# Kernel tuning notes

Measured on AMD Instinct MI355X. Metric: run time of the kernel, lower is better.

## Reference

```python
import jax, jax.numpy as jnp
import numpy as np

B, S, E = 20, 4096, 256
BLOCK = 128
LEFT, RIGHT = 1, 1


def setup_inputs() -> dict:
    key = jax.random.key(0)
    ks = jax.random.split(key, 6)
    x = jax.random.normal(ks[0], (B, S, E), dtype=jnp.float32)
    scale = 0.02
    Wq = jax.random.normal(ks[1], (E, E), dtype=jnp.float32) * scale
    Wk = jax.random.normal(ks[2], (E, E), dtype=jnp.float32) * scale
    Wv = jax.random.normal(ks[3], (E, E), dtype=jnp.float32) * scale
    Wo = jax.random.normal(ks[4], (E, E), dtype=jnp.float32) * scale
    bo = jnp.zeros((E,), dtype=jnp.float32)
    return {"x": x, "Wq": Wq, "Wk": Wk, "Wv": Wv, "Wo": Wo, "bo": bo}


def _block_context(blocks, left, right):
    # blocks: [B, nb, bs, E] -> [B, nb, (left+right+1)*bs, E]
    b, nb, bs, e = blocks.shape
    w = left + right + 1
    padded = jnp.pad(blocks, ((0, 0), (left, right), (0, 0), (0, 0)))
    idx = jnp.arange(nb)[:, None] + jnp.arange(w)[None, :]  # [nb, w]
    ctx = padded[:, idx]  # [B, nb, w, bs, E]
    return ctx.reshape(b, nb, w * bs, e)


def reference(x, Wq, Wk, Wv, Wo, bo):
    b, s, e = x.shape
    nb = s // BLOCK
    q = x @ Wq
    k = x @ Wk
    v = x @ Wv
    qb = q.reshape(b, nb, BLOCK, e)
    kb = k.reshape(b, nb, BLOCK, e)
    vb = v.reshape(b, nb, BLOCK, e)
    kc = _block_context(kb, LEFT, RIGHT)  # [B, nb, ctx, E]
    vc = _block_context(vb, LEFT, RIGHT)
    logits = jnp.einsum('bnqd,bnkd->bnqk', qb, kc) / jnp.sqrt(jnp.float32(e))
    attn = jax.nn.softmax(logits, axis=-1)
    out = jnp.einsum('bnqk,bnkd->bnqd', attn, vc)  # [B, nb, bs, E]
    # Faithful to TF: TensorArray.stack() -> [nb, B, bs, E], then reshape to [B, S, E]
    out = jnp.transpose(out, (1, 0, 2, 3)).reshape(b, s, e)
    return out @ Wo + bo
```

## Files before the change

kernel.cpp:

```cpp
#include <hip/hip_runtime.h>
#include <stdint.h>

#define B_   20
#define S_   4096
#define E_   256
#define NB_  32
#define M_   (B_ * S_)

#define OFF_Q   41943040ull
#define OFF_K   83886080ull
#define OFF_V   125829120ull
#define OFF_WT  167772160ull

typedef __attribute__((ext_vector_type(4))) float f32x4;
typedef __attribute__((ext_vector_type(8))) short short8;
typedef __attribute__((ext_vector_type(4))) float float4v;
typedef __attribute__((ext_vector_type(4))) unsigned short us4;

__device__ __forceinline__ unsigned short f2bf(float f) {
  unsigned int u = __builtin_bit_cast(unsigned int, f);
  u += 0x7FFFu + ((u >> 16) & 1u);
  return (unsigned short)(u >> 16);
}

__device__ __forceinline__ void glds16(const void* g, void* l) {
  __builtin_amdgcn_global_load_lds(
      (const __attribute__((address_space(1))) unsigned int*)g,
      (__attribute__((address_space(3))) unsigned int*)l, 16, 0, 0);
}

__global__ void k_convert_x(const float* __restrict__ x, unsigned short* __restrict__ xb) {
  size_t id = (size_t)blockIdx.x * 256 + threadIdx.x;
  float4v v = *(const float4v*)(x + id * 4);
  us4 o;
  o[0] = f2bf(v[0]); o[1] = f2bf(v[1]); o[2] = f2bf(v[2]); o[3] = f2bf(v[3]);
  *(us4*)(xb + id * 4) = o;
}

__global__ void k_convert_w(const float* __restrict__ Wq, const float* __restrict__ Wk,
                            const float* __restrict__ Wv, const float* __restrict__ Wo,
                            unsigned short* __restrict__ WT) {
  const float* src = (blockIdx.x == 0) ? Wq : (blockIdx.x == 1) ? Wk
                   : (blockIdx.x == 2) ? Wv : Wo;
  unsigned short* dst = WT + (size_t)blockIdx.x * 65536;
  int n = threadIdx.x;
  for (int k = 0; k < 256; ++k)
    dst[n * 256 + k] = f2bf(src[k * 256 + n]);
}

template <bool QKV>
__global__ __launch_bounds__(256, 2) void k_gemm(const unsigned short* __restrict__ A,
                                                 const unsigned short* __restrict__ WT,
                                                 void* __restrict__ out,
                                                 unsigned short* __restrict__ vT,
                                                 const float* __restrict__ bias) {
  __shared__ char Alds[2][16384];
  __shared__ char Blds[2][16384];
  const int nct = QKV ? 6 : 2;
  int g = blockIdx.x;
  int xcd = g & 7, idx = g >> 3;
  int rt = xcd * 80 + idx / nct;
  int ct = idx % nct;
  int mat = QKV ? (ct >> 1) : 3;
  int col0 = (ct & 1) * 128;

  int tid = threadIdx.x, w = tid >> 6, l = tid & 63;
  int wr = (w >> 1) * 64, wc = (w & 1) * 64;
  int hi16 = (l >> 4) * 16;

  const char* Ab = (const char*)A + (size_t)rt * 128 * 512;
  const char* Bb = (const char*)(WT + (size_t)mat * 65536) + (size_t)col0 * 512;

  auto STAGE = [&](int bufi, int s) {
    int k0b = s * 128;
#pragma unroll
    for (int j8 = 0; j8 < 4; ++j8) {
      int d = (j8 * 256 + tid) * 16;
      int row = d >> 7;
      int cx = (d & 127) ^ ((row & 7) << 4);
      glds16(Ab + (size_t)row * 512 + k0b + cx, Alds[bufi] + d);
      glds16(Bb + (size_t)row * 512 + k0b + cx, Blds[bufi] + d);
    }
  };

  f32x4 acc[4][4] = {};
  STAGE(0, 0);

  for (int s = 0; s < 4; ++s) {
    int cur = s & 1;
    if (s < 3) {
      STAGE(cur ^ 1, s + 1);
      asm volatile("s_waitcnt vmcnt(8)" ::: "memory");
    } else {
      asm volatile("s_waitcnt vmcnt(0)" ::: "memory");
    }
    __builtin_amdgcn_sched_barrier(0);
    __builtin_amdgcn_s_barrier();
#pragma unroll
    for (int ks = 0; ks < 2; ++ks) {
      short8 a[4], bb[4];
#pragma unroll
      for (int i = 0; i < 4; ++i) {
        int ra = wr + 16 * i + (l & 15);
        a[i] = *(const short8*)(Alds[cur] + ra * 128 + ((ks * 64 + hi16) ^ ((ra & 7) << 4)));
        int rb = wc + 16 * i + (l & 15);
        bb[i] = *(const short8*)(Blds[cur] + rb * 128 + ((rb & 7) << 4 ^ (ks * 64 + hi16)));
      }
      __builtin_amdgcn_s_setprio(1);
#pragma unroll
      for (int i = 0; i < 4; ++i)
#pragma unroll
        for (int j = 0; j < 4; ++j)
          acc[i][j] = __builtin_amdgcn_mfma_f32_16x16x32_bf16(a[i], bb[j], acc[i][j], 0, 0, 0);
      __builtin_amdgcn_s_setprio(0);
    }
    asm volatile("s_waitcnt lgkmcnt(0)" ::: "memory");
    __builtin_amdgcn_sched_barrier(0);
    __builtin_amdgcn_s_barrier();
  }

  if constexpr (QKV) {
    if (mat < 2) {
      unsigned short* oq = (unsigned short*)out + (size_t)mat * M_ * 256;
#pragma unroll
      for (int i = 0; i < 4; ++i)
#pragma unroll
        for (int j = 0; j < 4; ++j)
#pragma unroll
          for (int r = 0; r < 4; ++r) {
            int row = rt * 128 + wr + 16 * i + (l >> 4) * 4 + r;
            int col = col0 + wc + 16 * j + (l & 15);
            oq[(size_t)row * 256 + col] = f2bf(acc[i][j][r]);
          }
    } else {
#pragma unroll
      for (int i = 0; i < 4; ++i) {
        int row0 = rt * 128 + wr + 16 * i + (l >> 4) * 4;
        int b = row0 >> 12, s0 = row0 & 4095;
#pragma unroll
        for (int j = 0; j < 4; ++j) {
          int col = col0 + wc + 16 * j + (l & 15);
          us4 o;
#pragma unroll
          for (int r = 0; r < 4; ++r) o[r] = f2bf(acc[i][j][r]);
          *(us4*)(vT + ((size_t)(b * 256 + col) << 12) + s0) = o;
        }
      }
    }
  } else {
    float* of = (float*)out;
#pragma unroll
    for (int i = 0; i < 4; ++i)
#pragma unroll
      for (int j = 0; j < 4; ++j)
#pragma unroll
        for (int r = 0; r < 4; ++r) {
          int row = rt * 128 + wr + 16 * i + (l >> 4) * 4 + r;
          int col = col0 + wc + 16 * j + (l & 15);
          of[(size_t)row * 256 + col] = acc[i][j][r] + bias[col];
        }
  }
}

__global__ __launch_bounds__(256, 2) void k_attn(const unsigned short* __restrict__ q,
                                                 const unsigned short* __restrict__ k,
                                                 const unsigned short* __restrict__ vT,
                                                 unsigned short* __restrict__ ob) {
  __shared__ char kb2[2][32768];
  __shared__ char pl[64 * 144];

  int g = blockIdx.x;
  int xcd = g & 7, idx = g >> 3;
  int nbid = xcd * 80 + (idx >> 1);
  int half = idx & 1;
  int b = nbid >> 5, n = nbid & 31;
  int tid = threadIdx.x, w = tid >> 6, l = tid & 63;
  int hi16 = (l >> 4) * 16;

  int rowbase = b * 4096 + n * 128 + half * 64 + w * 16;
  const char* qrow = (const char*)q + (size_t)(rowbase + (l & 15)) * 512;
  short8 qf[8];
#pragma unroll
  for (int ks = 0; ks < 8; ++ks) qf[ks] = *(const short8*)(qrow + ks * 64 + hi16);

  f32x4 zero4 = {0.f, 0.f, 0.f, 0.f};
  f32x4 oacc[16];
#pragma unroll
  for (int fj = 0; fj < 16; ++fj) oacc[fj] = zero4;
  float einit = (n == 0 || n == 31) ? 8.0f : 0.0f;
  float dsum[4] = {einit, einit, einit, einit};

  const char* kbase = (const char*)k + (size_t)b * 4096 * 512;
  const char* vtb   = (const char*)vT + (size_t)b * 256 * 8192;

  int c0 = (n == 0) ? 2 : 0;
  int c1 = (n == 31) ? 3 : 5;
  int P = (c1 - c0 + 1) * 2;

  auto STAGE = [&](int bufi, int p) {
    int c = c0 + (p >> 1);
    int kg = (n + (c >> 1) - 1) * 128 + (c & 1) * 64;
    char* dst = kb2[bufi];
    if ((p & 1) == 0) {
#pragma unroll
      for (int j8 = 0; j8 < 8; ++j8) {
        int d = (j8 * 256 + tid) * 16;
        int key = d >> 9;
        int f2 = (d & 511) ^ ((key & 7) << 4);
        glds16(kbase + (size_t)(kg + key) * 512 + f2, dst + d);
      }
    } else {
#pragma unroll
      for (int j8 = 0; j8 < 8; ++j8) {
        int d = (j8 * 256 + tid) * 16;
        int feat = d >> 7;
        int kx = (d & 127) ^ ((feat & 7) << 4);
        glds16(vtb + (size_t)feat * 8192 + (size_t)kg * 2 + kx, dst + d);
      }
    }
  };

  STAGE(0, 0);

  for (int p = 0; p < P; ++p) {
    int cur = p & 1;
    if (p + 1 < P) {
      STAGE(cur ^ 1, p + 1);
      asm volatile("s_waitcnt vmcnt(8)" ::: "memory");
    } else {
      asm volatile("s_waitcnt vmcnt(0)" ::: "memory");
    }
    __builtin_amdgcn_sched_barrier(0);
    __builtin_amdgcn_s_barrier();

    const char* kv = kb2[cur];
    if ((p & 1) == 0) {
#pragma unroll
      for (int j = 0; j < 4; ++j) {
        f32x4 s = zero4;
        int key = 16 * j + (l & 15);
        int kb0 = key * 512, km = (key & 7) << 4;
        __builtin_amdgcn_s_setprio(1);
#pragma unroll
        for (int ks = 0; ks < 8; ++ks) {
          short8 kf = *(const short8*)(kv + kb0 + ((ks * 64 + hi16) ^ km));
          s = __builtin_amdgcn_mfma_f32_16x16x32_bf16(qf[ks], kf, s, 0, 0, 0);
        }
        __builtin_amdgcn_s_setprio(0);
#pragma unroll
        for (int r = 0; r < 4; ++r) {
          float pv = __expf(s[r] * 0.0625f);
          dsum[r] += pv;
          int prow = w * 16 + (l >> 4) * 4 + r;
          *(unsigned short*)(pl + prow * 144 + key * 2) = f2bf(pv);
        }
      }
    } else {
#pragma unroll
      for (int ks2 = 0; ks2 < 2; ++ks2) {
        short8 pa = *(const short8*)(pl + (w * 16 + (l & 15)) * 144 + ks2 * 64 + hi16);
        __builtin_amdgcn_s_setprio(1);
#pragma unroll
        for (int fj = 0; fj < 16; ++fj) {
          int feat = 16 * fj + (l & 15);
          short8 vf = *(const short8*)(kv + feat * 128 + ((ks2 * 64 + hi16) ^ ((feat & 7) << 4)));
          oacc[fj] = __builtin_amdgcn_mfma_f32_16x16x32_bf16(pa, vf, oacc[fj], 0, 0, 0);
        }
        __builtin_amdgcn_s_setprio(0);
      }
    }
    asm volatile("s_waitcnt lgkmcnt(0)" ::: "memory");
    __builtin_amdgcn_sched_barrier(0);
    __builtin_amdgcn_s_barrier();
  }

#pragma unroll
  for (int r = 0; r < 4; ++r) {
    float t = dsum[r];
    t += __shfl_xor(t, 1); t += __shfl_xor(t, 2);
    t += __shfl_xor(t, 4); t += __shfl_xor(t, 8);
    dsum[r] = 1.0f / t;
  }

  int orow0 = n * 2560 + b * 128 + half * 64 + w * 16 + (l >> 4) * 4;
#pragma unroll
  for (int fj = 0; fj < 16; ++fj) {
    int col = 16 * fj + (l & 15);
#pragma unroll
    for (int r = 0; r < 4; ++r)
      ob[(size_t)(orow0 + r) * 256 + col] = f2bf(oacc[fj][r] * dsum[r]);
  }
}

extern "C" void kernel_launch(void* const* d_in, const int* in_sizes, int n_in,
                              void* d_out, int out_size, void* d_ws, size_t ws_size,
                              hipStream_t stream) {
  (void)in_sizes; (void)n_in; (void)out_size; (void)ws_size;
  const float* x  = (const float*)d_in[0];
  const float* Wq = (const float*)d_in[1];
  const float* Wk = (const float*)d_in[2];
  const float* Wv = (const float*)d_in[3];
  const float* Wo = (const float*)d_in[4];
  const float* bo = (const float*)d_in[5];

  char* ws = (char*)d_ws;
  unsigned short* xb = (unsigned short*)ws;
  unsigned short* qb = (unsigned short*)(ws + OFF_Q);
  unsigned short* kb = (unsigned short*)(ws + OFF_K);
  unsigned short* vT = (unsigned short*)(ws + OFF_V);
  unsigned short* WT = (unsigned short*)(ws + OFF_WT);

  k_convert_x<<<20480, 256, 0, stream>>>(x, xb);
  k_convert_w<<<4, 256, 0, stream>>>(Wq, Wk, Wv, Wo, WT);
  k_gemm<true><<<3840, 256, 0, stream>>>(xb, WT, (void*)qb, vT, nullptr);
  k_attn<<<1280, 256, 0, stream>>>(qb, kb, vT, xb);
  k_gemm<false><<<1280, 256, 0, stream>>>(xb, WT, d_out, nullptr, bo);
}
```

Before: 310.4 us.

## Fuse output projection into attention kernel and stage GEMM epilogue through LDS

The Wo projection and bias add move into the attention kernel. Each block writes its normalized attention output tile to LDS as bf16, streams Wo^T in chunks, and runs MFMAs to produce the final fp32 output directly. This removes the third GEMM launch and the bf16 round-trip of the attention output through global memory. The QKV GEMM epilogue now writes through a swizzled LDS tile and stores coalesced 16-byte rows, including for the transposed V layout. In exchange, the attention kernel gains extra registers (a second 16-fragment accumulator) and extra LDS traffic and barriers, which may reduce occupancy.

Measured after the change: 331.2 us. +6.7%, slower.

```diff
diff --git a/kernel.cpp b/kernel.cpp
--- a/kernel.cpp
+++ b/kernel.cpp
@@ -48,20 +48,17 @@
     dst[n * 256 + k] = f2bf(src[k * 256 + n]);
 }
 
-template <bool QKV>
 __global__ __launch_bounds__(256, 2) void k_gemm(const unsigned short* __restrict__ A,
                                                  const unsigned short* __restrict__ WT,
-                                                 void* __restrict__ out,
-                                                 unsigned short* __restrict__ vT,
-                                                 const float* __restrict__ bias) {
+                                                 unsigned short* __restrict__ qk,
+                                                 unsigned short* __restrict__ vT) {
   __shared__ char Alds[2][16384];
   __shared__ char Blds[2][16384];
-  const int nct = QKV ? 6 : 2;
   int g = blockIdx.x;
   int xcd = g & 7, idx = g >> 3;
-  int rt = xcd * 80 + idx / nct;
-  int ct = idx % nct;
-  int mat = QKV ? (ct >> 1) : 3;
+  int rt = xcd * 80 + idx / 6;
+  int ct = idx % 6;
+  int mat = ct >> 1;
   int col0 = (ct & 1) * 128;
 
   int tid = threadIdx.x, w = tid >> 6, l = tid & 63;
@@ -119,53 +116,55 @@
     __builtin_amdgcn_s_barrier();
   }
 
-  if constexpr (QKV) {
-    if (mat < 2) {
-      unsigned short* oq = (unsigned short*)out + (size_t)mat * M_ * 256;
-#pragma unroll
-      for (int i = 0; i < 4; ++i)
-#pragma unroll
-        for (int j = 0; j < 4; ++j)
-#pragma unroll
-          for (int r = 0; r < 4; ++r) {
-            int row = rt * 128 + wr + 16 * i + (l >> 4) * 4 + r;
-            int col = col0 + wc + 16 * j + (l & 15);
-            oq[(size_t)row * 256 + col] = f2bf(acc[i][j][r]);
-          }
-    } else {
-#pragma unroll
-      for (int i = 0; i < 4; ++i) {
-        int row0 = rt * 128 + wr + 16 * i + (l >> 4) * 4;
-        int b = row0 >> 12, s0 = row0 & 4095;
-#pragma unroll
-        for (int j = 0; j < 4; ++j) {
-          int col = col0 + wc + 16 * j + (l & 15);
-          us4 o;
-#pragma unroll
-          for (int r = 0; r < 4; ++r) o[r] = f2bf(acc[i][j][r]);
-          *(us4*)(vT + ((size_t)(b * 256 + col) << 12) + s0) = o;
-        }
-      }
-    }
+  char* E = &Alds[0][0];
+  if (mat < 2) {
+#pragma unroll
+    for (int i = 0; i < 4; ++i)
+#pragma unroll
+      for (int j = 0; j < 4; ++j)
+#pragma unroll
+        for (int r = 0; r < 4; ++r) {
+          int rowL = wr + 16 * i + (l >> 4) * 4 + r;
+          int colL = wc + 16 * j + (l & 15);
+          *(unsigned short*)(E + rowL * 256 + ((2 * colL) ^ ((rowL & 7) << 4))) =
+              f2bf(acc[i][j][r]);
+        }
   } else {
-    float* of = (float*)out;
 #pragma unroll
     for (int i = 0; i < 4; ++i)
 #pragma unroll
       for (int j = 0; j < 4; ++j)
 #pragma unroll
         for (int r = 0; r < 4; ++r) {
-          int row = rt * 128 + wr + 16 * i + (l >> 4) * 4 + r;
-          int col = col0 + wc + 16 * j + (l & 15);
-          of[(size_t)row * 256 + col] = acc[i][j][r] + bias[col];
-        }
+          int rowL = wr + 16 * i + (l >> 4) * 4 + r;
+          int colL = wc + 16 * j + (l & 15);
+          *(unsigned short*)(E + colL * 256 + ((2 * rowL) ^ ((colL & 7) << 4))) =
+              f2bf(acc[i][j][r]);
+        }
+  }
+  __syncthreads();
+  int o = tid >> 1, h = tid & 1;
+  char* gdst;
+  if (mat < 2) {
+    gdst = (char*)(qk + (size_t)mat * M_ * 256) + (size_t)(rt * 128 + o) * 512 +
+           (size_t)col0 * 2 + h * 128;
+  } else {
+    int b = rt >> 5;
+    gdst = (char*)vT + (size_t)(b * 256 + col0 + o) * 8192 + (size_t)(rt & 31) * 256 + h * 128;
+  }
+#pragma unroll
+  for (int i = 0; i < 8; ++i) {
+    short8 v = *(const short8*)(E + o * 256 + ((h * 128 + i * 16) ^ ((o & 7) << 4)));
+    *(short8*)(gdst + i * 16) = v;
   }
 }
 
 __global__ __launch_bounds__(256, 2) void k_attn(const unsigned short* __restrict__ q,
                                                  const unsigned short* __restrict__ k,
                                                  const unsigned short* __restrict__ vT,
-                                                 unsigned short* __restrict__ ob) {
+                                                 const unsigned short* __restrict__ WT,
+                                                 const float* __restrict__ bo,
+                                                 float* __restrict__ out) {
   __shared__ char kb2[2][32768];
   __shared__ char pl[64 * 144];
 
@@ -192,6 +191,7 @@
 
   const char* kbase = (const char*)k + (size_t)b * 4096 * 512;
   const char* vtb   = (const char*)vT + (size_t)b * 256 * 8192;
+  const char* woT   = (const char*)(WT + 3 * 65536);
 
   int c0 = (n == 0) ? 2 : 0;
   int c1 = (n == 31) ? 3 : 5;
@@ -282,13 +282,66 @@
     dsum[r] = 1.0f / t;
   }
 
-  int orow0 = n * 2560 + b * 128 + half * 64 + w * 16 + (l >> 4) * 4;
+  char* OL = kb2[0];
 #pragma unroll
   for (int fj = 0; fj < 16; ++fj) {
-    int col = 16 * fj + (l & 15);
+    int c2 = 2 * (16 * fj + (l & 15));
+#pragma unroll
+    for (int r = 0; r < 4; ++r) {
+      int qr = w * 16 + (l >> 4) * 4 + r;
+      *(unsigned short*)(OL + qr * 512 + (c2 ^ ((qr & 7) << 4))) =
+          f2bf(oacc[fj][r] * dsum[r]);
+    }
+  }
+
+  auto STAGE_WO = [&](int kc) {
+#pragma unroll
+    for (int j8 = 0; j8 < 8; ++j8) {
+      int d = (j8 * 256 + tid) * 16;
+      int nrow = d >> 7;
+      int kx = (d & 127) ^ ((nrow & 7) << 4);
+      glds16(woT + (size_t)nrow * 512 + kc * 128 + kx, kb2[1] + d);
+    }
+  };
+
+  f32x4 acc2[16];
+#pragma unroll
+  for (int j = 0; j < 16; ++j) acc2[j] = zero4;
+
+  STAGE_WO(0);
+  for (int kc = 0; kc < 4; ++kc) {
+    asm volatile("s_waitcnt vmcnt(0)" ::: "memory");
+    __builtin_amdgcn_sched_barrier(0);
+    __builtin_amdgcn_s_barrier();
+#pragma unroll
+    for (int kstep = 0; kstep < 2; ++kstep) {
+      int qr = w * 16 + (l & 15);
+      short8 af = *(const short8*)(OL + qr * 512 +
+                    ((kc * 128 + kstep * 64 + hi16) ^ ((qr & 7) << 4)));
+      __builtin_amdgcn_s_setprio(1);
+#pragma unroll
+      for (int j = 0; j < 16; ++j) {
+        int nr = 16 * j + (l & 15);
+        short8 bf = *(const short8*)(kb2[1] + nr * 128 +
+                      ((kstep * 64 + hi16) ^ ((nr & 7) << 4)));
+        acc2[j] = __builtin_amdgcn_mfma_f32_16x16x32_bf16(af, bf, acc2[j], 0, 0, 0);
+      }
+      __builtin_amdgcn_s_setprio(0);
+    }
+    asm volatile("s_waitcnt lgkmcnt(0)" ::: "memory");
+    __builtin_amdgcn_sched_barrier(0);
+    __builtin_amdgcn_s_barrier();
+    if (kc < 3) STAGE_WO(kc + 1);
+  }
+
+  int f0 = n * 2560 + b * 128 + half * 64 + w * 16 + (l >> 4) * 4;
+#pragma unroll
+  for (int j = 0; j < 16; ++j) {
+    int col = 16 * j + (l & 15);
+    float bj = bo[col];
 #pragma unroll
     for (int r = 0; r < 4; ++r)
-      ob[(size_t)(orow0 + r) * 256 + col] = f2bf(oacc[fj][r] * dsum[r]);
+      out[(size_t)(f0 + r) * 256 + col] = acc2[j][r] + bj;
   }
 }
 
@@ -312,7 +365,6 @@
 
   k_convert_x<<<20480, 256, 0, stream>>>(x, xb);
   k_convert_w<<<4, 256, 0, stream>>>(Wq, Wk, Wv, Wo, WT);
-  k_gemm<true><<<3840, 256, 0, stream>>>(xb, WT, (void*)qb, vT, nullptr);
-  k_attn<<<1280, 256, 0, stream>>>(qb, kb, vT, xb);
-  k_gemm<false><<<1280, 256, 0, stream>>>(xb, WT, d_out, nullptr, bo);
-}
+  k_gemm<<<3840, 256, 0, stream>>>(xb, WT, qb, vT);
+  k_attn<<<1280, 256, 0, stream>>>(qb, kb, vT, WT, bo, (float*)d_out);
+}
```
